# Kernel tuning notes

Hardware: AMD Instinct MI355X
Metric: run time of the kernel (lower is better)

Reference implementation:

```python
import jax, jax.numpy as jnp
import numpy as np

K = 4            # number of candidate kernels in Dynamic_conv2d
TEMP = 34.0      # softmax temperature (default in Dynamic_conv2d)
C = 64           # channel


def _dyn_conv(x, w, fc1_w, fc2_w, fc2_b, pad, dil):
    """Dynamic_conv2d forward.
    x: [B,Cin,H,W]; w: [K,Cout,Cin,k,k]; fc1_w: [hid,Cin]; fc2_w: [K,hid]; fc2_b: [K].
    """
    pooled = x.mean(axis=(2, 3))                                   # [B,Cin] adaptive avg pool
    h = jax.nn.relu(jnp.einsum('bc,hc->bh', pooled, fc1_w))        # [B,hid]
    logits = jnp.einsum('bh,kh->bk', h, fc2_w) + fc2_b             # [B,K]
    att = jax.nn.softmax(logits / TEMP, axis=-1)                   # [B,K]
    agg_w = jnp.einsum('bk,koihw->boihw', att, w)                  # per-sample kernel [B,Cout,Cin,k,k]

    def conv_one(xi, wi):
        return jax.lax.conv_general_dilated(
            xi[None], wi, window_strides=(1, 1),
            padding=[(pad, pad), (pad, pad)], rhs_dilation=(dil, dil),
            dimension_numbers=('NCHW', 'OIHW', 'NCHW'))[0]

    return jax.vmap(conv_one)(x, agg_w)                            # [B,Cout,H,W]


def _leaky(v):
    return jnp.where(v >= 0, v, 0.1 * v)


def _mk_params(key, cin, cout):
    hid = int(cin * 0.25) + 1
    k1, k2, k3, k4 = jax.random.split(key, 4)
    scale = np.sqrt(2.0 / (cin * 9)).astype(np.float32)
    w = jax.random.normal(k1, (K, cout, cin, 3, 3), jnp.float32) * scale
    fc1 = jax.random.normal(k2, (hid, cin), jnp.float32) * np.sqrt(2.0 / cin).astype(np.float32)
    fc2w = jax.random.normal(k3, (K, hid), jnp.float32) * np.sqrt(2.0 / hid).astype(np.float32)
    fc2b = jnp.zeros((K,), jnp.float32)
    return w, fc1, fc2w, fc2b


def setup_inputs() -> dict:
    key = jax.random.key(0)
    ks = jax.random.split(key, 5)
    x = jax.random.normal(ks[0], (16, C, 128, 128), jnp.float32)
    out = {'x': x}
    for i, (kk, cin) in enumerate(zip(ks[1:4], [C, C, C]), start=1):
        w, fc1, fc2w, fc2b = _mk_params(kk, cin, C)
        out[f'w{i}'], out[f'fc1_{i}'], out[f'fc2w_{i}'], out[f'fc2b_{i}'] = w, fc1, fc2w, fc2b
    w, fc1, fc2w, fc2b = _mk_params(ks[4], 3 * C, C)
    out['wt'], out['fc1_t'], out['fc2w_t'], out['fc2b_t'] = w, fc1, fc2w, fc2b
    return out


def reference(x, w1, fc1_1, fc2w_1, fc2b_1, w2, fc1_2, fc2w_2, fc2b_2,
              w3, fc1_3, fc2w_3, fc2b_3, wt, fc1_t, fc2w_t, fc2b_t):
    b1 = _leaky(_dyn_conv(x, w1, fc1_1, fc2w_1, fc2b_1, pad=1, dil=1))
    b2 = _leaky(_dyn_conv(x, w2, fc1_2, fc2w_2, fc2b_2, pad=2, dil=2))
    b3 = _leaky(_dyn_conv(x, w3, fc1_3, fc2w_3, fc2b_3, pad=4, dil=4))
    cat = jnp.concatenate([b1, b2, b3], axis=1)                    # [B,3C,H,W]
    return x + _dyn_conv(cat, wt, fc1_t, fc2w_t, fc2b_t, pad=1, dil=1)
```

## Files before the change

### kernel.cpp

```cpp
#include <hip/hip_runtime.h>
#include <hip/hip_bf16.h>

typedef __hip_bfloat16 bf16;
typedef __attribute__((ext_vector_type(4))) float f32x4;
typedef __attribute__((ext_vector_type(8))) short bf16x8;
typedef __attribute__((ext_vector_type(4))) short s16x4;

#define BB 16
#define HH 128
#define WW 128
#define HWSZ (HH*WW)
#define XH 136
#define XW 136
#define XPAD 4
#define CHH 130
#define CWD 130
#define CPAD 1
#define CATC 192

__device__ __forceinline__ void zero_border_body(bf16* __restrict__ base, int HP, int WP,
                                                 int PAD, int Cdim, int slots)
{
    int cg8 = Cdim >> 3;
    int per_b = slots * cg8;
    int idx = blockIdx.x * 256 + threadIdx.x;
    if (idx >= BB * per_b) return;
    int b = idx / per_b;
    int rem = idx - b * per_b;
    int slot = rem / cg8;
    int cg = rem - slot * cg8;
    int top = PAD * WP;
    int h, w;
    if (slot < top)            { h = slot / WP;            w = slot % WP; }
    else if (slot < 2 * top)   { int s = slot - top;       h = HP - PAD + s / WP; w = s % WP; }
    else {
        int s = slot - 2 * top;
        int row = s / (2 * PAD), t = s - row * (2 * PAD);
        h = PAD + row;
        w = (t < PAD) ? t : (WP - 2 * PAD + t);
    }
    bf16x8 z = {0,0,0,0,0,0,0,0};
    *(bf16x8*)(base + (((size_t)b * HP + h) * WP + w) * Cdim + cg * 8) = z;
}

__global__ void init_borders(bf16* __restrict__ xT, bf16* __restrict__ catT)
{
    if (blockIdx.y == 0) zero_border_body(xT,   XH,  XW,  XPAD, 64,   2112);
    else                 zero_border_body(catT, CHH, CWD, CPAD, CATC, 516);
}

__global__ __launch_bounds__(256)
void transpose_pad_pool_x(const float* __restrict__ x, bf16* __restrict__ xT,
                          float* __restrict__ pooledx)
{
    __shared__ float tile[128 * 65];
    const int h = blockIdx.x, b = blockIdx.y;
    const int t = threadIdx.x;
    const int w  = t & 127;
    const int chalf = t >> 7;

    const float* xb = x + (((size_t)b * 64) * HH + h) * WW + w;
    #pragma unroll
    for (int it = 0; it < 32; ++it) {
        int c = it * 2 + chalf;
        tile[w * 65 + c] = xb[(size_t)c * HWSZ];
    }
    __syncthreads();

    bf16* dst = xT + (((size_t)b * XH + (h + XPAD)) * XW + XPAD) * 64;
    #pragma unroll
    for (int it = 0; it < 4; ++it) {
        int v  = t + it * 256;
        int ww = v >> 3;
        int c0 = (v & 7) * 8;
        const float* src = tile + ww * 65 + c0;
        bf16x8 pk;
        #pragma unroll
        for (int j = 0; j < 8; ++j)
            pk[j] = __builtin_bit_cast(short, __float2bfloat16(src[j]));
        *(bf16x8*)(dst + (size_t)ww * 64 + c0) = pk;
    }

    if (t < 64) {
        float s = 0.f;
        #pragma unroll 4
        for (int ww = 0; ww < 128; ++ww) s += tile[ww * 65 + t];
        atomicAdd(pooledx + b * 64 + t, s);
    }
}

__device__ __forceinline__ void attn_body(int b, const float* pooled, int Cin,
                                          const float* fc1, int hid,
                                          const float* fc2w, const float* fc2b,
                                          float* att, float* sp, float* sh, float* slg)
{
    for (int c = threadIdx.x; c < Cin; c += 64) sp[c] = pooled[b * Cin + c];
    __syncthreads();
    int j = threadIdx.x;
    if (j < hid) {
        float s = 0.f;
        const float4* f4 = (const float4*)(fc1 + (size_t)j * Cin);
        for (int c4 = 0; c4 < Cin / 4; ++c4) {
            float4 v = f4[c4];
            s += v.x * sp[c4*4+0] + v.y * sp[c4*4+1] + v.z * sp[c4*4+2] + v.w * sp[c4*4+3];
        }
        sh[j] = s > 0.f ? s * (1.0f / 16384.0f) : 0.f;
    }
    __syncthreads();
    int k = threadIdx.x;
    if (k < 4) {
        float s = fc2b[k];
        for (int jj = 0; jj < hid; ++jj) s += fc2w[k * hid + jj] * sh[jj];
        slg[k] = s * (1.0f / 34.0f);
    }
    __syncthreads();
    if (threadIdx.x == 0) {
        float m = fmaxf(fmaxf(slg[0], slg[1]), fmaxf(slg[2], slg[3]));
        float e0 = expf(slg[0]-m), e1 = expf(slg[1]-m), e2 = expf(slg[2]-m), e3 = expf(slg[3]-m);
        float inv = 1.0f / (e0+e1+e2+e3);
        att[b*4+0] = e0*inv; att[b*4+1] = e1*inv; att[b*4+2] = e2*inv; att[b*4+3] = e3*inv;
    }
}

__global__ void attention3(const float* __restrict__ pooled,
                           const float* f1a, const float* f2a, const float* ba, float* aa,
                           const float* f1b, const float* f2b, const float* bb, float* ab,
                           const float* f1c, const float* f2c, const float* bc, float* ac)
{
    __shared__ float sp[192], sh[64], slg[4];
    int br = blockIdx.y;
    const float* fc1  = br == 0 ? f1a : br == 1 ? f1b : f1c;
    const float* fc2w = br == 0 ? f2a : br == 1 ? f2b : f2c;
    const float* fc2b = br == 0 ? ba  : br == 1 ? bb  : bc;
    float* att        = br == 0 ? aa  : br == 1 ? ab  : ac;
    attn_body(blockIdx.x, pooled, 64, fc1, 17, fc2w, fc2b, att, sp, sh, slg);
}

__global__ void attention_one(const float* __restrict__ pooled, int Cin,
                              const float* __restrict__ fc1, int hid,
                              const float* __restrict__ fc2w,
                              const float* __restrict__ fc2b, float* __restrict__ att)
{
    __shared__ float sp[192], sh[64], slg[4];
    attn_body(blockIdx.x, pooled, Cin, fc1, hid, fc2w, fc2b, att, sp, sh, slg);
}

template<int CIN, bool PERM>
__device__ __forceinline__ void aggw_body(const float* __restrict__ w,
                                          const float* __restrict__ att,
                                          bf16* __restrict__ out, float* wl)
{
    constexpr int C9 = CIN * 9;
    constexpr int NS = (CIN / 32) * 9;
    const int co = blockIdx.x, b = blockIdx.y;
    const int src = PERM ? ((co & 15) * 4 + (co >> 4)) : co;
    for (int i = threadIdx.x; i < 4 * C9; i += 256) {
        int k = i / C9, rem = i - k * C9;
        wl[i] = w[((size_t)k * 64 + src) * C9 + rem];
    }
    __syncthreads();
    float a0 = att[b*4+0], a1 = att[b*4+1], a2 = att[b*4+2], a3 = att[b*4+3];
    const int m = co >> 4, l15 = co & 15;
    char* ob = (char*)out + (size_t)b * NS * 4096;
    for (int t = threadIdx.x; t < NS * 32; t += 256) {
        int s = t >> 5, rem = t & 31;
        int gg = rem >> 3, j = rem & 7;
        int chunk = s / 9, tap = s - chunk * 9;
        int ci = chunk * 32 + gg * 8 + j;
        float v = a0 * wl[ci*9 + tap] + a1 * wl[C9 + ci*9 + tap]
                + a2 * wl[2*C9 + ci*9 + tap] + a3 * wl[3*C9 + ci*9 + tap];
        *(bf16*)(ob + ((size_t)((s*4 + m) * 64 + (gg*16 + l15))) * 16 + j * 2) = __float2bfloat16(v);
    }
}

__global__ void aggw_frag3(const float* __restrict__ w1, const float* __restrict__ att1, bf16* o1,
                           const float* __restrict__ w2, const float* __restrict__ att2, bf16* o2,
                           const float* __restrict__ w3, const float* __restrict__ att3, bf16* o3)
{
    __shared__ float wl[4 * 64 * 9];
    int z = blockIdx.z;
    if (z == 0)      aggw_body<64, true>(w1, att1, o1, wl);
    else if (z == 1) aggw_body<64, true>(w2, att2, o2, wl);
    else             aggw_body<64, true>(w3, att3, o3, wl);
}

__global__ void aggw_frag_t(const float* __restrict__ w, const float* __restrict__ att,
                            bf16* __restrict__ out)
{
    __shared__ float wl[4 * 192 * 9];
    aggw_body<192, false>(w, att, out, wl);
}

template<int DIL, int CIN, bool RESID>
__device__ __forceinline__ void conv_core(
    int b, int hb, int wt,
    const bf16* __restrict__ inT, int HPd, int WPd, int PAD,
    const bf16* __restrict__ aggwF,
    const float* __restrict__ xres, float* __restrict__ outf,
    bf16* __restrict__ catT, int catbase, float* __restrict__ poolc,
    char* lds, float* sco)
{
    constexpr int NCHUNK = CIN / 32;
    constexpr int SLOTS  = 64 + 2 * DIL;
    constexpr int ROWB   = SLOTS * 64;
    constexpr int XBYTES = 10 * ROWB;
    constexpr int XSEG   = (XBYTES + 1023) / 1024;
    constexpr int ABYTES = 36864;
    constexpr int MAXT   = (XSEG + 7) / 8;

    const int r  = hb % DIL;
    const int q  = hb / DIL;
    const int tid  = threadIdx.x;
    const int wv   = tid >> 6;
    const int lane = tid & 63;
    const int n16  = lane & 15;
    const int g    = lane >> 4;

    const char* inB = (const char*)inT;
    const char* awB = (const char*)aggwF + (size_t)b * (NCHUNK * ABYTES);

    if (!RESID && tid < 64) sco[tid] = 0.f;

    int baddr[12];
    #pragma unroll
    for (int nt = 0; nt < 4; ++nt)
        #pragma unroll
        for (int kw = 0; kw < 3; ++kw)
            baddr[nt*3+kw] = wv * ROWB + g * (SLOTS * 16)
                             + (nt * 16 + n16 + kw * DIL) * 16;

    int xoff[MAXT];
    #pragma unroll
    for (int t = 0; t < MAXT; ++t) {
        int i = wv + 8 * t;
        xoff[t] = 0;
        if (i < XSEG) {
            int o = i * 1024 + lane * 16;
            if (o < XBYTES) {
                int row  = o / ROWB;
                int rem  = o - row * ROWB;
                int g2   = rem / (SLOTS * 16);
                int slot = (rem - g2 * (SLOTS * 16)) >> 4;
                int h_in = (q * 8 + row - 1) * DIL + r;
                xoff[t] = ((b * HPd + PAD + h_in) * WPd + (PAD + wt * 64 - DIL + slot)) * (CIN * 2)
                          + g2 * 16;
            }
        }
    }

    auto stage = [&](int c) {
        #pragma unroll
        for (int t = 0; t < MAXT; ++t) {
            int i = wv + 8 * t;
            if (i >= XSEG) break;
            __builtin_amdgcn_global_load_lds(
                (const __attribute__((address_space(1))) void*)(inB + (size_t)(xoff[t] + c * 64)),
                (__attribute__((address_space(3))) void*)(lds + i * 1024), 16, 0, 0);
        }
    };

    f32x4 acc[4][4];
    #pragma unroll
    for (int nt = 0; nt < 4; ++nt)
        #pragma unroll
        for (int m = 0; m < 4; ++m) { f32x4 z = {0.f,0.f,0.f,0.f}; acc[nt][m] = z; }

    for (int c = 0; c < NCHUNK; ++c) {
        stage(c);
        __syncthreads();
        const char* awC = awB + (size_t)c * ABYTES + (size_t)lane * 16;
        #pragma unroll 3
        for (int tap = 0; tap < 9; ++tap) {
            const int kh = tap / 3, kw = tap - kh * 3;
            bf16x8 a[4];
            #pragma unroll
            for (int m = 0; m < 4; ++m)
                a[m] = *(const bf16x8*)(awC + (size_t)((tap * 4 + m) * 1024));
            #pragma unroll
            for (int nt = 0; nt < 4; ++nt) {
                const bf16x8 bfr = *(const bf16x8*)(lds + baddr[nt * 3 + kw] + kh * ROWB);
                #pragma unroll
                for (int m = 0; m < 4; ++m)
                    acc[nt][m] = __builtin_amdgcn_mfma_f32_16x16x32_bf16(a[m], bfr, acc[nt][m], 0, 0, 0);
            }
        }
        __syncthreads();
    }

    const int h_out = (q * 8 + wv) * DIL + r;
    if (RESID) {
        #pragma unroll
        for (int nt = 0; nt < 4; ++nt) {
            int w_out = wt * 64 + nt * 16 + n16;
            #pragma unroll
            for (int m = 0; m < 4; ++m) {
                int co = m * 16 + g * 4;
                size_t base = (((size_t)b * 64 + co) * HH + h_out) * WW + w_out;
                #pragma unroll
                for (int qq = 0; qq < 4; ++qq) {
                    size_t idx = base + (size_t)qq * HWSZ;
                    outf[idx] = xres[idx] + acc[nt][m][qq];
                }
            }
        }
    } else {
        float csum[4][4];
        #pragma unroll
        for (int m = 0; m < 4; ++m)
            #pragma unroll
            for (int qq = 0; qq < 4; ++qq) csum[m][qq] = 0.f;
        #pragma unroll
        for (int nt = 0; nt < 4; ++nt) {
            int w_out = wt * 64 + nt * 16 + n16;
            char* dst = (char*)(catT + (((size_t)b * CHH + (CPAD + h_out)) * CWD + (CPAD + w_out)) * CATC
                                + catbase) + g * 32;
            float lv[4][4];
            #pragma unroll
            for (int m = 0; m < 4; ++m)
                #pragma unroll
                for (int qq = 0; qq < 4; ++qq) {
                    float v = acc[nt][m][qq];
                    v = v >= 0.f ? v : 0.1f * v;
                    lv[m][qq] = v;
                    csum[m][qq] += v;
                }
            bf16x8 lo, hi;
            #pragma unroll
            for (int j = 0; j < 8; ++j) {
                lo[j] = __builtin_bit_cast(short, __float2bfloat16(lv[j & 3][j >> 2]));
                hi[j] = __builtin_bit_cast(short, __float2bfloat16(lv[j & 3][2 + (j >> 2)]));
            }
            *(bf16x8*)(dst)      = lo;
            *(bf16x8*)(dst + 16) = hi;
        }
        #pragma unroll
        for (int m = 0; m < 4; ++m)
            #pragma unroll
            for (int qq = 0; qq < 4; ++qq) {
                float v = csum[m][qq];
                v += __shfl_xor(v, 1, 64);
                v += __shfl_xor(v, 2, 64);
                v += __shfl_xor(v, 4, 64);
                v += __shfl_xor(v, 8, 64);
                if (n16 == 0) atomicAdd(&sco[g * 16 + qq * 4 + m], v);
            }
        __syncthreads();
        if (tid < 64) atomicAdd(poolc + b * CATC + catbase + tid, sco[tid]);
    }
}

__global__ __launch_bounds__(512, 4)
void conv_branch3(const bf16* __restrict__ xT,
                  const bf16* __restrict__ aggF1, const bf16* __restrict__ aggF2,
                  const bf16* __restrict__ aggF3,
                  bf16* __restrict__ catT, float* __restrict__ poolc)
{
    constexpr int SCOO = 46080;
    __shared__ __align__(1024) char lds[SCOO + 256];
    float* sco = (float*)(lds + SCOO);

    const int bid  = blockIdx.x;
    const int xcd  = bid & 7;
    const int j    = bid >> 3;
    const int b    = 2 * xcd + (j >= 96 ? 1 : 0);
    const int u    = j % 96;
    const int band = u / 24;
    const int v    = u % 24;
    const int br   = v % 3;
    const int t2   = v / 3;
    const int wt   = t2 & 1;
    const int hb   = band * 4 + (t2 >> 1);

    if (br == 0)
        conv_core<1, 64, false>(b, hb, wt, xT, XH, XW, XPAD,
                                aggF1, nullptr, nullptr, catT, 0, poolc, lds, sco);
    else if (br == 1)
        conv_core<2, 64, false>(b, hb, wt, xT, XH, XW, XPAD,
                                aggF2, nullptr, nullptr, catT, 64, poolc, lds, sco);
    else
        conv_core<4, 64, false>(b, hb, wt, xT, XH, XW, XPAD,
                                aggF3, nullptr, nullptr, catT, 128, poolc, lds, sco);
}

__global__ __launch_bounds__(512, 4)
void conv_final(const bf16* __restrict__ catT, const bf16* __restrict__ aggFt,
                const float* __restrict__ x, float* __restrict__ out)
{
    constexpr int XSEGF = (10 * 66 * 64 + 1023) / 1024;
    constexpr int SCOO  = XSEGF * 1024;
    __shared__ __align__(1024) char lds[SCOO + 256];

    const int bid = blockIdx.x;
    const int xcd = bid & 7;
    const int j   = bid >> 3;
    const int b   = 2 * xcd + (j >= 32 ? 1 : 0);
    const int u   = j % 32;
    const int wt  = u & 1;
    const int hb  = u >> 1;

    conv_core<1, 192, true>(b, hb, wt, catT, CHH, CWD, CPAD,
                            aggFt, x, out, nullptr, 0, nullptr, lds, (float*)(lds + SCOO));
}

extern "C" void kernel_launch(void* const* d_in, const int* in_sizes, int n_in,
                              void* d_out, int out_size, void* d_ws, size_t ws_size,
                              hipStream_t stream) {
    const float* x      = (const float*)d_in[0];
    const float* w1     = (const float*)d_in[1];
    const float* fc1_1  = (const float*)d_in[2];
    const float* fc2w_1 = (const float*)d_in[3];
    const float* fc2b_1 = (const float*)d_in[4];
    const float* w2     = (const float*)d_in[5];
    const float* fc1_2  = (const float*)d_in[6];
    const float* fc2w_2 = (const float*)d_in[7];
    const float* fc2b_2 = (const float*)d_in[8];
    const float* w3     = (const float*)d_in[9];
    const float* fc1_3  = (const float*)d_in[10];
    const float* fc2w_3 = (const float*)d_in[11];
    const float* fc2b_3 = (const float*)d_in[12];
    const float* wt     = (const float*)d_in[13];
    const float* fc1_t  = (const float*)d_in[14];
    const float* fc2w_t = (const float*)d_in[15];
    const float* fc2b_t = (const float*)d_in[16];
    float* out = (float*)d_out;
    (void)in_sizes; (void)n_in; (void)out_size; (void)ws_size;

    char* ws = (char*)d_ws;
    auto alloc = [&](size_t bytes) { char* p = ws; ws += (bytes + 255) & ~(size_t)255; return p; };

    bf16*  aggF1   = (bf16*)alloc((size_t)BB * 18 * 4096);
    bf16*  aggF2   = (bf16*)alloc((size_t)BB * 18 * 4096);
    bf16*  aggF3   = (bf16*)alloc((size_t)BB * 18 * 4096);
    bf16*  aggFt   = (bf16*)alloc((size_t)BB * 54 * 4096);
    float* pooledx = (float*)alloc(BB * 64 * 4);
    float* pooledc = (float*)alloc(BB * 192 * 4);
    float* att1    = (float*)alloc(BB * 4 * 4);
    float* att2    = (float*)alloc(BB * 4 * 4);
    float* att3    = (float*)alloc(BB * 4 * 4);
    float* attt    = (float*)alloc(BB * 4 * 4);
    alloc(65536);
    const size_t XT_BYTES  = (size_t)BB * XH * XW * 64 * 2;
    bf16* xT   = (bf16*)alloc(XT_BYTES);
    alloc(65536);
    const size_t CAT_BYTES = (size_t)BB * CHH * CWD * CATC * 2;
    bf16* catT = (bf16*)alloc(CAT_BYTES);
    alloc(65536);

    hipMemsetAsync(pooledx, 0, BB * 64 * 4, stream);
    hipMemsetAsync(pooledc, 0, BB * 192 * 4, stream);

    init_borders<<<dim3(1056, 2), 256, 0, stream>>>(xT, catT);

    transpose_pad_pool_x<<<dim3(128, 16), 256, 0, stream>>>(x, xT, pooledx);

    attention3<<<dim3(16, 3), 64, 0, stream>>>(pooledx,
        fc1_1, fc2w_1, fc2b_1, att1,
        fc1_2, fc2w_2, fc2b_2, att2,
        fc1_3, fc2w_3, fc2b_3, att3);

    aggw_frag3<<<dim3(64, 16, 3), 256, 0, stream>>>(w1, att1, aggF1,
                                                    w2, att2, aggF2,
                                                    w3, att3, aggF3);

    conv_branch3<<<1536, 512, 0, stream>>>(xT, aggF1, aggF2, aggF3, catT, pooledc);

    attention_one<<<16, 64, 0, stream>>>(pooledc, CATC, fc1_t, 49, fc2w_t, fc2b_t, attt);
    aggw_frag_t<<<dim3(64, 16), 256, 0, stream>>>(wt, attt, aggFt);

    conv_final<<<512, 512, 0, stream>>>(catT, aggFt, x, out);
}
```

Baseline: 232.8 us.

## Give final conv its own double-buffered kernel with smaller 4-row tiles

The final 192-channel convolution gets its own dedicated kernel instead of reusing the shared conv_core template. It now uses 256-thread blocks covering 4 output rows, twice as many blocks, and double-buffered LDS staging via global_load_lds so the next 32-channel chunk loads while MFMAs run on the current one. The aim is to hide global-to-LDS latency and improve occupancy and wave-level parallelism. The cost is more halo reloading per output row, since 4-row tiles read 6 input rows, plus larger per-block LDS use for two buffers.

```diff
diff --git a/kernel.cpp b/kernel.cpp
--- a/kernel.cpp
+++ b/kernel.cpp
@@ -191,12 +191,11 @@
     aggw_body<192, false>(w, att, out, wl);
 }
 
-template<int DIL, int CIN, bool RESID>
+template<int DIL, int CIN>
 __device__ __forceinline__ void conv_core(
     int b, int hb, int wt,
     const bf16* __restrict__ inT, int HPd, int WPd, int PAD,
     const bf16* __restrict__ aggwF,
-    const float* __restrict__ xres, float* __restrict__ outf,
     bf16* __restrict__ catT, int catbase, float* __restrict__ poolc,
     char* lds, float* sco)
 {
@@ -219,7 +218,7 @@
     const char* inB = (const char*)inT;
     const char* awB = (const char*)aggwF + (size_t)b * (NCHUNK * ABYTES);
 
-    if (!RESID && tid < 64) sco[tid] = 0.f;
+    if (tid < 64) sco[tid] = 0.f;
 
     int baddr[12];
     #pragma unroll
@@ -288,65 +287,48 @@
     }
 
     const int h_out = (q * 8 + wv) * DIL + r;
-    if (RESID) {
-        #pragma unroll
-        for (int nt = 0; nt < 4; ++nt) {
-            int w_out = wt * 64 + nt * 16 + n16;
-            #pragma unroll
-            for (int m = 0; m < 4; ++m) {
-                int co = m * 16 + g * 4;
-                size_t base = (((size_t)b * 64 + co) * HH + h_out) * WW + w_out;
-                #pragma unroll
-                for (int qq = 0; qq < 4; ++qq) {
-                    size_t idx = base + (size_t)qq * HWSZ;
-                    outf[idx] = xres[idx] + acc[nt][m][qq];
-                }
-            }
-        }
-    } else {
-        float csum[4][4];
-        #pragma unroll
-        for (int m = 0; m < 4; ++m)
-            #pragma unroll
-            for (int qq = 0; qq < 4; ++qq) csum[m][qq] = 0.f;
-        #pragma unroll
-        for (int nt = 0; nt < 4; ++nt) {
-            int w_out = wt * 64 + nt * 16 + n16;
-            char* dst = (char*)(catT + (((size_t)b * CHH + (CPAD + h_out)) * CWD + (CPAD + w_out)) * CATC
-                                + catbase) + g * 32;
-            float lv[4][4];
-            #pragma unroll
-            for (int m = 0; m < 4; ++m)
-                #pragma unroll
-                for (int qq = 0; qq < 4; ++qq) {
-                    float v = acc[nt][m][qq];
-                    v = v >= 0.f ? v : 0.1f * v;
-                    lv[m][qq] = v;
-                    csum[m][qq] += v;
-                }
-            bf16x8 lo, hi;
-            #pragma unroll
-            for (int j = 0; j < 8; ++j) {
-                lo[j] = __builtin_bit_cast(short, __float2bfloat16(lv[j & 3][j >> 2]));
-                hi[j] = __builtin_bit_cast(short, __float2bfloat16(lv[j & 3][2 + (j >> 2)]));
-            }
-            *(bf16x8*)(dst)      = lo;
-            *(bf16x8*)(dst + 16) = hi;
-        }
+    float csum[4][4];
+    #pragma unroll
+    for (int m = 0; m < 4; ++m)
+        #pragma unroll
+        for (int qq = 0; qq < 4; ++qq) csum[m][qq] = 0.f;
+    #pragma unroll
+    for (int nt = 0; nt < 4; ++nt) {
+        int w_out = wt * 64 + nt * 16 + n16;
+        char* dst = (char*)(catT + (((size_t)b * CHH + (CPAD + h_out)) * CWD + (CPAD + w_out)) * CATC
+                            + catbase) + g * 32;
+        float lv[4][4];
         #pragma unroll
         for (int m = 0; m < 4; ++m)
             #pragma unroll
             for (int qq = 0; qq < 4; ++qq) {
-                float v = csum[m][qq];
-                v += __shfl_xor(v, 1, 64);
-                v += __shfl_xor(v, 2, 64);
-                v += __shfl_xor(v, 4, 64);
-                v += __shfl_xor(v, 8, 64);
-                if (n16 == 0) atomicAdd(&sco[g * 16 + qq * 4 + m], v);
+                float v = acc[nt][m][qq];
+                v = v >= 0.f ? v : 0.1f * v;
+                lv[m][qq] = v;
+                csum[m][qq] += v;
             }
-        __syncthreads();
-        if (tid < 64) atomicAdd(poolc + b * CATC + catbase + tid, sco[tid]);
-    }
+        bf16x8 lo, hi;
+        #pragma unroll
+        for (int j = 0; j < 8; ++j) {
+            lo[j] = __builtin_bit_cast(short, __float2bfloat16(lv[j & 3][j >> 2]));
+            hi[j] = __builtin_bit_cast(short, __float2bfloat16(lv[j & 3][2 + (j >> 2)]));
+        }
+        *(bf16x8*)(dst)      = lo;
+        *(bf16x8*)(dst + 16) = hi;
+    }
+    #pragma unroll
+    for (int m = 0; m < 4; ++m)
+        #pragma unroll
+        for (int qq = 0; qq < 4; ++qq) {
+            float v = csum[m][qq];
+            v += __shfl_xor(v, 1, 64);
+            v += __shfl_xor(v, 2, 64);
+            v += __shfl_xor(v, 4, 64);
+            v += __shfl_xor(v, 8, 64);
+            if (n16 == 0) atomicAdd(&sco[g * 16 + qq * 4 + m], v);
+        }
+    __syncthreads();
+    if (tid < 64) atomicAdd(poolc + b * CATC + catbase + tid, sco[tid]);
 }
 
 __global__ __launch_bounds__(512, 4)
@@ -372,34 +354,123 @@
     const int hb   = band * 4 + (t2 >> 1);
 
     if (br == 0)
-        conv_core<1, 64, false>(b, hb, wt, xT, XH, XW, XPAD,
-                                aggF1, nullptr, nullptr, catT, 0, poolc, lds, sco);
+        conv_core<1, 64>(b, hb, wt, xT, XH, XW, XPAD, aggF1, catT, 0,   poolc, lds, sco);
     else if (br == 1)
-        conv_core<2, 64, false>(b, hb, wt, xT, XH, XW, XPAD,
-                                aggF2, nullptr, nullptr, catT, 64, poolc, lds, sco);
+        conv_core<2, 64>(b, hb, wt, xT, XH, XW, XPAD, aggF2, catT, 64,  poolc, lds, sco);
     else
-        conv_core<4, 64, false>(b, hb, wt, xT, XH, XW, XPAD,
-                                aggF3, nullptr, nullptr, catT, 128, poolc, lds, sco);
-}
-
-__global__ __launch_bounds__(512, 4)
+        conv_core<4, 64>(b, hb, wt, xT, XH, XW, XPAD, aggF3, catT, 128, poolc, lds, sco);
+}
+
+#define FF_ROWB 4224
+#define FF_XBY  25344
+#define FF_XSEG 25
+#define FF_BUFB 25600
+
+__global__ __launch_bounds__(256, 4)
 void conv_final(const bf16* __restrict__ catT, const bf16* __restrict__ aggFt,
                 const float* __restrict__ x, float* __restrict__ out)
 {
-    constexpr int XSEGF = (10 * 66 * 64 + 1023) / 1024;
-    constexpr int SCOO  = XSEGF * 1024;
-    __shared__ __align__(1024) char lds[SCOO + 256];
+    __shared__ __align__(1024) char lds[2 * FF_BUFB];
 
     const int bid = blockIdx.x;
     const int xcd = bid & 7;
     const int j   = bid >> 3;
-    const int b   = 2 * xcd + (j >= 32 ? 1 : 0);
-    const int u   = j % 32;
+    const int b   = 2 * xcd + (j >= 64 ? 1 : 0);
+    const int u   = j & 63;
     const int wt  = u & 1;
     const int hb  = u >> 1;
 
-    conv_core<1, 192, true>(b, hb, wt, catT, CHH, CWD, CPAD,
-                            aggFt, x, out, nullptr, 0, nullptr, lds, (float*)(lds + SCOO));
+    const int tid  = threadIdx.x;
+    const int wv   = tid >> 6;
+    const int lane = tid & 63;
+    const int n16  = lane & 15;
+    const int g    = lane >> 4;
+
+    const char* inB = (const char*)catT;
+    const char* awB = (const char*)aggFt + (size_t)b * (6 * 36864);
+
+    int baddr[12];
+    #pragma unroll
+    for (int nt = 0; nt < 4; ++nt)
+        #pragma unroll
+        for (int kw = 0; kw < 3; ++kw)
+            baddr[nt*3+kw] = wv * FF_ROWB + g * (66 * 16) + (nt * 16 + n16 + kw) * 16;
+
+    int xoff[7];
+    #pragma unroll
+    for (int t = 0; t < 7; ++t) {
+        int i = wv + 4 * t;
+        xoff[t] = 0;
+        if (i < FF_XSEG) {
+            int o = i * 1024 + lane * 16;
+            if (o < FF_XBY) {
+                int row  = o / FF_ROWB;
+                int rem  = o - row * FF_ROWB;
+                int g2   = rem / (66 * 16);
+                int slot = (rem - g2 * (66 * 16)) >> 4;
+                int h_in = hb * 4 + row - 1;
+                xoff[t] = ((b * CHH + CPAD + h_in) * CWD + (CPAD + wt * 64 - 1 + slot)) * (CATC * 2)
+                          + g2 * 16;
+            }
+        }
+    }
+
+    auto stage = [&](int c, int pb) {
+        #pragma unroll
+        for (int t = 0; t < 7; ++t) {
+            int i = wv + 4 * t;
+            if (i >= FF_XSEG) break;
+            __builtin_amdgcn_global_load_lds(
+                (const __attribute__((address_space(1))) void*)(inB + (size_t)(xoff[t] + c * 64)),
+                (__attribute__((address_space(3))) void*)(lds + pb + i * 1024), 16, 0, 0);
+        }
+    };
+
+    f32x4 acc[4][4];
+    #pragma unroll
+    for (int nt = 0; nt < 4; ++nt)
+        #pragma unroll
+        for (int m = 0; m < 4; ++m) { f32x4 z = {0.f,0.f,0.f,0.f}; acc[nt][m] = z; }
+
+    stage(0, 0);
+    __syncthreads();
+    for (int c = 0; c < 6; ++c) {
+        const int p = (c & 1) * FF_BUFB;
+        if (c < 5) stage(c + 1, FF_BUFB - p);
+        const char* awC = awB + (size_t)c * 36864 + (size_t)lane * 16;
+        #pragma unroll 3
+        for (int tap = 0; tap < 9; ++tap) {
+            const int kh = tap / 3, kw = tap - kh * 3;
+            bf16x8 a[4];
+            #pragma unroll
+            for (int m = 0; m < 4; ++m)
+                a[m] = *(const bf16x8*)(awC + (size_t)((tap * 4 + m) * 1024));
+            #pragma unroll
+            for (int nt = 0; nt < 4; ++nt) {
+                const bf16x8 bfr = *(const bf16x8*)(lds + p + baddr[nt * 3 + kw] + kh * FF_ROWB);
+                #pragma unroll
+                for (int m = 0; m < 4; ++m)
+                    acc[nt][m] = __builtin_amdgcn_mfma_f32_16x16x32_bf16(a[m], bfr, acc[nt][m], 0, 0, 0);
+            }
+        }
+        __syncthreads();
+    }
+
+    const int h_out = hb * 4 + wv;
+    #pragma unroll
+    for (int nt = 0; nt < 4; ++nt) {
+        int w_out = wt * 64 + nt * 16 + n16;
+        #pragma unroll
+        for (int m = 0; m < 4; ++m) {
+            int co = m * 16 + g * 4;
+            size_t base = (((size_t)b * 64 + co) * HH + h_out) * WW + w_out;
+            #pragma unroll
+            for (int qq = 0; qq < 4; ++qq) {
+                size_t idx = base + (size_t)qq * HWSZ;
+                out[idx] = x[idx] + acc[nt][m][qq];
+            }
+        }
+    }
 }
 
 extern "C" void kernel_launch(void* const* d_in, const int* in_sizes, int n_in,
@@ -467,5 +538,5 @@
     attention_one<<<16, 64, 0, stream>>>(pooledc, CATC, fc1_t, 49, fc2w_t, fc2b_t, attt);
     aggw_frag_t<<<dim3(64, 16), 256, 0, stream>>>(wt, attt, aggFt);
 
-    conv_final<<<512, 512, 0, stream>>>(catT, aggFt, x, out);
-}
+    conv_final<<<1024, 256, 0, stream>>>(catT, aggFt, x, out);
+}
```

Result: slower. 265.2 us (+13.9%).
